# Kernel optimization log

Hardware: AMD Instinct MI355X
Metric: run time of the kernel (lower is better)

## Reference

```python
import jax, jax.numpy as jnp
import numpy as np

HEADS = 16
DIM_HEAD = 64
SCALE = DIM_HEAD ** -0.5


def setup_inputs() -> dict:
    key = jax.random.key(0)
    k1, k2, k3 = jax.random.split(key, 3)
    B, N, C = 2, 2048, 1024
    inner = HEADS * DIM_HEAD  # 1024
    x = jax.random.normal(k1, (B, N, C), dtype=jnp.float32)
    w_qkv = jax.random.normal(k2, (C, 3 * inner), dtype=jnp.float32) * (C ** -0.5)
    w_proj = jax.random.normal(k3, (inner, C), dtype=jnp.float32) * (inner ** -0.5)
    b_proj = jnp.zeros((C,), dtype=jnp.float32)
    return {"x": x, "w_qkv": w_qkv, "w_proj": w_proj, "b_proj": b_proj}


def reference(x, w_qkv, w_proj, b_proj):
    B, N, C = x.shape
    qkv = x @ w_qkv  # [B, N, 3*inner]
    qkv = qkv.reshape(B, N, 3, HEADS, DIM_HEAD)
    qkv = jnp.transpose(qkv, (2, 0, 3, 1, 4))  # [3, B, H, N, D]
    q, k, v = qkv[0], qkv[1], qkv[2]
    q = q * SCALE
    attn = jnp.einsum('bhnd,bhmd->bhnm', q, k)  # [B, H, N, N]
    attn = jax.nn.softmax(attn, axis=-1)
    out = jnp.einsum('bhnm,bhmd->bhnd', attn, v)  # [B, H, N, D]
    out = jnp.transpose(out, (0, 2, 1, 3)).reshape(B, N, HEADS * DIM_HEAD)
    return out @ w_proj + b_proj
```

## Files before the change

### kernel.cpp

```cpp
#include <hip/hip_runtime.h>
#include <hip/hip_bf16.h>
#include <cstdint>
#include <cstddef>

static constexpr int BATCH = 2;
static constexpr int SEQ   = 2048;
static constexpr int CDIM  = 1024;
static constexpr int ROWS  = BATCH * SEQ;
static constexpr int QKVN  = 3 * CDIM;

typedef short bf16x8 __attribute__((ext_vector_type(8)));
typedef short bf16x4 __attribute__((ext_vector_type(4)));
typedef float f32x4  __attribute__((ext_vector_type(4)));

__device__ inline short f2bf(float f) {
    union { float f; unsigned u; } v; v.f = f;
    unsigned u = v.u;
    u += 0x7fffu + ((u >> 16) & 1u);
    return (short)(u >> 16);
}

__device__ inline unsigned pk_bf16(float a, float b) {
    union { float f; unsigned u; } ua, ub;
    ua.f = a; ub.f = b;
    unsigned xa = ua.u + 0x7fffu + ((ua.u >> 16) & 1u);
    unsigned xb = ub.u + 0x7fffu + ((ub.u >> 16) & 1u);
    return __builtin_amdgcn_perm(xb, xa, 0x07060302);
}

__device__ inline void glds16(const short* g, short* l) {
    __builtin_amdgcn_global_load_lds(
        (const __attribute__((address_space(1))) void*)g,
        (__attribute__((address_space(3))) void*)l, 16, 0, 0);
}

__device__ inline f32x4 mfma16_bf16(bf16x4 a, bf16x4 b, f32x4 c) {
#if __has_builtin(__builtin_amdgcn_mfma_f32_16x16x16bf16_1k)
    return __builtin_amdgcn_mfma_f32_16x16x16bf16_1k(a, b, c, 0, 0, 0);
#else
    asm("v_mfma_f32_16x16x16_bf16 %0, %1, %2, %0" : "+v"(c) : "v"(a), "v"(b));
    return c;
#endif
}

__global__ __launch_bounds__(256) void cvt_f32_bf16(const float* __restrict__ in,
                                                    short* __restrict__ out, int n4) {
    int i = blockIdx.x * 256 + threadIdx.x;
    if (i >= n4) return;
    float4 f = ((const float4*)in)[i];
    uint2 o;
    o.x = pk_bf16(f.x, f.y);
    o.y = pk_bf16(f.z, f.w);
    ((uint2*)out)[i] = o;
}

__global__ __launch_bounds__(256) void cvt_transpose(const float* __restrict__ in,
                                                     short* __restrict__ out, int R, int C,
                                                     float scale, int srows) {
    __shared__ float tile[32][33];
    int tx = threadIdx.x & 31, ty = threadIdx.x >> 5;
    int r0 = blockIdx.y * 32, c0 = blockIdx.x * 32;
    #pragma unroll
    for (int i = 0; i < 4; i++)
        tile[ty + i * 8][tx] = in[(size_t)(r0 + ty + i * 8) * C + c0 + tx];
    __syncthreads();
    #pragma unroll
    for (int i = 0; i < 4; i++) {
        int orow = c0 + ty + i * 8;
        float sc = (orow < srows) ? scale : 1.0f;
        out[(size_t)orow * R + r0 + tx] = f2bf(tile[tx][ty + i * 8] * sc);
    }
}

__global__ __launch_bounds__(256) void v_transpose(const short* __restrict__ qkv,
                                                   short* __restrict__ vTg) {
    __shared__ short tile[32][33];
    int bh = blockIdx.z, b = bh >> 4, h = bh & 15;
    int n0 = blockIdx.x * 32, d0 = blockIdx.y * 32;
    int tx = threadIdx.x & 31, ty = threadIdx.x >> 5;
    const short* src = qkv + (size_t)(b * SEQ) * QKVN + 2048 + h * 64;
    #pragma unroll
    for (int i = 0; i < 4; i++)
        tile[ty + i * 8][tx] = src[(size_t)(n0 + ty + i * 8) * QKVN + d0 + tx];
    __syncthreads();
    short* dst = vTg + (size_t)bh * (64 * SEQ);
    #pragma unroll
    for (int i = 0; i < 4; i++)
        dst[(size_t)(d0 + ty + i * 8) * SEQ + n0 + tx] = tile[tx][ty + i * 8];
}

template<int BF16OUT>
__global__ __launch_bounds__(256) void gemm_bt(const short* __restrict__ A,
                                               const short* __restrict__ Bt,
                                               void* __restrict__ C,
                                               const float* __restrict__ bias,
                                               int M, int N, int K) {
    __shared__ __align__(16) short As[128 * 32];
    __shared__ __align__(16) short Bs[128 * 32];

    const int t = threadIdx.x, wave = t >> 6, lane = t & 63;
    const int l15 = lane & 15, quad = lane >> 4;
    const int wr = wave >> 1, wc = wave & 1;
    const int m0 = blockIdx.y * 128, n0 = blockIdx.x * 128;

    f32x4 acc[4][4] = {};

    const short* gA = A  + (size_t)(m0 + wave * 32 + (lane >> 2)) * K + (lane & 3) * 8;
    const short* gB = Bt + (size_t)(n0 + wave * 32 + (lane >> 2)) * K + (lane & 3) * 8;
    short* lA = &As[wave * 32 * 32];
    short* lB = &Bs[wave * 32 * 32];

    for (int k0 = 0; k0 < K; k0 += 32) {
        glds16(gA + k0,          lA);
        glds16(gA + 16 * K + k0, lA + 512);
        glds16(gB + k0,          lB);
        glds16(gB + 16 * K + k0, lB + 512);
        __syncthreads();

        bf16x8 af[4], bf[4];
        #pragma unroll
        for (int i = 0; i < 4; i++)
            af[i] = *(const bf16x8*)&As[(wr * 64 + i * 16 + l15) * 32 + quad * 8];
        #pragma unroll
        for (int j = 0; j < 4; j++)
            bf[j] = *(const bf16x8*)&Bs[(wc * 64 + j * 16 + l15) * 32 + quad * 8];
        #pragma unroll
        for (int i = 0; i < 4; i++)
            #pragma unroll
            for (int j = 0; j < 4; j++)
                acc[i][j] = __builtin_amdgcn_mfma_f32_16x16x32_bf16(af[i], bf[j], acc[i][j], 0, 0, 0);
        __syncthreads();
    }

    #pragma unroll
    for (int i = 0; i < 4; i++) {
        #pragma unroll
        for (int j = 0; j < 4; j++) {
            #pragma unroll
            for (int r = 0; r < 4; r++) {
                int row = m0 + wr * 64 + i * 16 + quad * 4 + r;
                int col = n0 + wc * 64 + j * 16 + l15;
                float v = acc[i][j][r];
                if (BF16OUT) ((short*)C)[(size_t)row * N + col] = f2bf(v);
                else         ((float*)C)[(size_t)row * N + col] = v + bias[col];
            }
        }
    }
}

static constexpr int KP      = 64 * 32;
static constexpr int VT_OFF  = 2 * KP;
static constexpr int LDV     = 72;
static constexpr int SMEM_SH = VT_OFF + 64 * LDV;

__global__ __launch_bounds__(256) void attn_kernel(const short* __restrict__ qkv,
                                                   const short* __restrict__ vTg,
                                                   short* __restrict__ attn_out) {
    __shared__ __align__(16) short smem[SMEM_SH];

    const int t = threadIdx.x, wave = t >> 6, lane = t & 63;
    const int l15 = lane & 15, quad = lane >> 4;
    const int bh = blockIdx.y, b = bh >> 4, h = bh & 15;
    const int q0 = blockIdx.x * 64;
    const size_t baseQ = (size_t)(b * SEQ) * QKVN + h * 64;

    const size_t qoff = baseQ + (size_t)(q0 + wave * 16 + l15) * QKVN + quad * 8;
    bf16x8 qf0 = *(const bf16x8*)&qkv[qoff];
    bf16x8 qf1 = *(const bf16x8*)&qkv[qoff + 32];

    const short* gK = qkv + baseQ + 1024
                    + (size_t)(wave * 16 + (lane >> 2)) * QKVN + (lane & 3) * 8;
    short* lK0 = smem + wave * 512;
    short* lK1 = smem + KP + wave * 512;

    const short* gV = vTg + (size_t)bh * (64 * SEQ);
    const int vd = t >> 3, vc = t & 7;

    float m_i = -INFINITY, l_i = 0.f;
    f32x4 ot[4] = {};

    for (int j0 = 0; j0 < SEQ; j0 += 64) {
        glds16(gK + (size_t)j0 * QKVN,      lK0);
        glds16(gK + (size_t)j0 * QKVN + 32, lK1);
        {
            int4 v0 = *(const int4*)&gV[(size_t)vd * SEQ + j0 + vc * 8];
            int4 v1 = *(const int4*)&gV[(size_t)(vd + 32) * SEQ + j0 + vc * 8];
            *(int4*)&smem[VT_OFF + vd * LDV + vc * 8]        = v0;
            *(int4*)&smem[VT_OFF + (vd + 32) * LDV + vc * 8] = v1;
        }
        __syncthreads();

        f32x4 s[4];
        #pragma unroll
        for (int sub = 0; sub < 4; sub++) {
            bf16x8 kf0 = *(const bf16x8*)&smem[(sub * 16 + l15) * 32 + quad * 8];
            bf16x8 kf1 = *(const bf16x8*)&smem[KP + (sub * 16 + l15) * 32 + quad * 8];
            f32x4 a = {};
            a = __builtin_amdgcn_mfma_f32_16x16x32_bf16(kf0, qf0, a, 0, 0, 0);
            a = __builtin_amdgcn_mfma_f32_16x16x32_bf16(kf1, qf1, a, 0, 0, 0);
            s[sub] = a;
        }

        float mx = fmaxf(fmaxf(fmaxf(s[0][0], s[0][1]), fmaxf(s[0][2], s[0][3])),
                         fmaxf(fmaxf(s[1][0], s[1][1]), fmaxf(s[1][2], s[1][3])));
        mx = fmaxf(mx, fmaxf(fmaxf(fmaxf(s[2][0], s[2][1]), fmaxf(s[2][2], s[2][3])),
                             fmaxf(fmaxf(s[3][0], s[3][1]), fmaxf(s[3][2], s[3][3]))));
        mx = fmaxf(mx, __shfl_xor(mx, 16));
        mx = fmaxf(mx, __shfl_xor(mx, 32));
        float mn = fmaxf(m_i, mx);
        if (!__all(mn == m_i)) {
            float alpha = __builtin_amdgcn_exp2f(m_i - mn);
            m_i = mn;
            l_i *= alpha;
            #pragma unroll
            for (int d = 0; d < 4; d++)
                #pragma unroll
                for (int r = 0; r < 4; r++) ot[d][r] *= alpha;
        }

        float rs = 0.f;
        #pragma unroll
        for (int sub = 0; sub < 4; sub++) {
            float p0 = __builtin_amdgcn_exp2f(s[sub][0] - m_i);
            float p1 = __builtin_amdgcn_exp2f(s[sub][1] - m_i);
            float p2 = __builtin_amdgcn_exp2f(s[sub][2] - m_i);
            float p3 = __builtin_amdgcn_exp2f(s[sub][3] - m_i);
            rs += (p0 + p1) + (p2 + p3);
            union { unsigned u[2]; bf16x4 v; } pu;
            pu.u[0] = pk_bf16(p0, p1);
            pu.u[1] = pk_bf16(p2, p3);
            #pragma unroll
            for (int d = 0; d < 4; d++) {
                bf16x4 vf = *(const bf16x4*)&smem[VT_OFF + (d * 16 + l15) * LDV
                                                 + sub * 16 + quad * 4];
                ot[d] = mfma16_bf16(vf, pu.v, ot[d]);
            }
        }
        rs += __shfl_xor(rs, 16);
        rs += __shfl_xor(rs, 32);
        l_i += rs;
        __syncthreads();
    }

    float inv = 1.0f / l_i;
    #pragma unroll
    for (int d = 0; d < 4; d++) {
        unsigned w0 = pk_bf16(ot[d][0] * inv, ot[d][1] * inv);
        unsigned w1 = pk_bf16(ot[d][2] * inv, ot[d][3] * inv);
        *(unsigned*)&smem[VT_OFF + (wave * 16 + l15) * LDV + d * 16 + quad * 4]     = w0;
        *(unsigned*)&smem[VT_OFF + (wave * 16 + l15) * LDV + d * 16 + quad * 4 + 2] = w1;
    }
    __syncthreads();
    {
        int row = t >> 3, ch = t & 7;
        #pragma unroll
        for (int p = 0; p < 2; p++) {
            int rr = row + p * 32;
            int4 v = *(const int4*)&smem[VT_OFF + rr * LDV + ch * 8];
            *(int4*)&attn_out[(size_t)(b * SEQ + q0 + rr) * CDIM + h * 64 + ch * 8] = v;
        }
    }
}

extern "C" void kernel_launch(void* const* d_in, const int* in_sizes, int n_in,
                              void* d_out, int out_size, void* d_ws, size_t ws_size,
                              hipStream_t stream) {
    const float* x      = (const float*)d_in[0];
    const float* w_qkv  = (const float*)d_in[1];
    const float* w_proj = (const float*)d_in[2];
    const float* b_proj = (const float*)d_in[3];
    float* out = (float*)d_out;

    char* ws = (char*)d_ws;
    short* x_bf    = (short*)(ws);
    short* wqkvT   = (short*)(ws + 8388608);
    short* wprojT  = (short*)(ws + 14680064);
    short* qkv_bf  = (short*)(ws + 16777216);
    short* attn_bf = (short*)(ws + 41943040);
    short* vTg     = x_bf;

    const float SMUL = 0.125f * 1.44269504088896340736f;

    cvt_f32_bf16<<<4096, 256, 0, stream>>>(x, x_bf, ROWS * CDIM / 4);
    cvt_transpose<<<dim3(QKVN / 32, CDIM / 32), 256, 0, stream>>>(w_qkv, wqkvT, CDIM, QKVN,
                                                                  SMUL, 1024);
    cvt_transpose<<<dim3(CDIM / 32, CDIM / 32), 256, 0, stream>>>(w_proj, wprojT, CDIM, CDIM,
                                                                  1.0f, 0);

    gemm_bt<1><<<dim3(QKVN / 128, ROWS / 128), 256, 0, stream>>>(
        x_bf, wqkvT, qkv_bf, nullptr, ROWS, QKVN, CDIM);

    v_transpose<<<dim3(SEQ / 32, 2, BATCH * 16), 256, 0, stream>>>(qkv_bf, vTg);

    attn_kernel<<<dim3(SEQ / 64, BATCH * 16), 256, 0, stream>>>(qkv_bf, vTg, attn_bf);

    gemm_bt<0><<<dim3(CDIM / 128, ROWS / 128), 256, 0, stream>>>(
        attn_bf, wprojT, out, b_proj, ROWS, CDIM, CDIM);
}
```

Measured before the change: 225.8 us.

## Widen attention KV tile, compute row sums via MFMA, shrink proj GEMM tile

The attention kernel now processes 128 keys per iteration instead of 64, which halves the number of loop iterations and barriers. The softmax row sum is now accumulated by an extra MFMA against a vector of ones instead of scalar adds and cross-lane shuffles. The output projection GEMM uses 64-row tiles, which doubles its block count so the small GEMM fills the GPU better. In exchange the kernel uses more shared memory and more registers for the larger score tile, and the row sum now comes from bf16-rounded probabilities.

```diff
diff --git a/kernel.cpp b/kernel.cpp
--- a/kernel.cpp
+++ b/kernel.cpp
@@ -89,43 +89,44 @@
         dst[(size_t)(d0 + ty + i * 8) * SEQ + n0 + tx] = tile[tx][ty + i * 8];
 }
 
-template<int BF16OUT>
+template<int BF16OUT, int MT>
 __global__ __launch_bounds__(256) void gemm_bt(const short* __restrict__ A,
                                                const short* __restrict__ Bt,
                                                void* __restrict__ C,
                                                const float* __restrict__ bias,
                                                int M, int N, int K) {
-    __shared__ __align__(16) short As[128 * 32];
+    constexpr int AF = MT / 32;
+    __shared__ __align__(16) short As[MT * 32];
     __shared__ __align__(16) short Bs[128 * 32];
 
     const int t = threadIdx.x, wave = t >> 6, lane = t & 63;
     const int l15 = lane & 15, quad = lane >> 4;
     const int wr = wave >> 1, wc = wave & 1;
-    const int m0 = blockIdx.y * 128, n0 = blockIdx.x * 128;
-
-    f32x4 acc[4][4] = {};
-
-    const short* gA = A  + (size_t)(m0 + wave * 32 + (lane >> 2)) * K + (lane & 3) * 8;
+    const int m0 = blockIdx.y * MT, n0 = blockIdx.x * 128;
+
+    f32x4 acc[AF][4] = {};
+
+    const short* gA = A  + (size_t)(m0 + wave * (MT / 4) + (lane >> 2)) * K + (lane & 3) * 8;
     const short* gB = Bt + (size_t)(n0 + wave * 32 + (lane >> 2)) * K + (lane & 3) * 8;
-    short* lA = &As[wave * 32 * 32];
+    short* lA = &As[wave * (MT / 4) * 32];
     short* lB = &Bs[wave * 32 * 32];
 
     for (int k0 = 0; k0 < K; k0 += 32) {
-        glds16(gA + k0,          lA);
-        glds16(gA + 16 * K + k0, lA + 512);
+        glds16(gA + k0, lA);
+        if constexpr (MT == 128) glds16(gA + 16 * K + k0, lA + 512);
         glds16(gB + k0,          lB);
         glds16(gB + 16 * K + k0, lB + 512);
         __syncthreads();
 
-        bf16x8 af[4], bf[4];
-        #pragma unroll
-        for (int i = 0; i < 4; i++)
-            af[i] = *(const bf16x8*)&As[(wr * 64 + i * 16 + l15) * 32 + quad * 8];
+        bf16x8 af[AF], bf[4];
+        #pragma unroll
+        for (int i = 0; i < AF; i++)
+            af[i] = *(const bf16x8*)&As[(wr * (MT / 2) + i * 16 + l15) * 32 + quad * 8];
         #pragma unroll
         for (int j = 0; j < 4; j++)
             bf[j] = *(const bf16x8*)&Bs[(wc * 64 + j * 16 + l15) * 32 + quad * 8];
         #pragma unroll
-        for (int i = 0; i < 4; i++)
+        for (int i = 0; i < AF; i++)
             #pragma unroll
             for (int j = 0; j < 4; j++)
                 acc[i][j] = __builtin_amdgcn_mfma_f32_16x16x32_bf16(af[i], bf[j], acc[i][j], 0, 0, 0);
@@ -133,12 +134,12 @@
     }
 
     #pragma unroll
-    for (int i = 0; i < 4; i++) {
+    for (int i = 0; i < AF; i++) {
         #pragma unroll
         for (int j = 0; j < 4; j++) {
             #pragma unroll
             for (int r = 0; r < 4; r++) {
-                int row = m0 + wr * 64 + i * 16 + quad * 4 + r;
+                int row = m0 + wr * (MT / 2) + i * 16 + quad * 4 + r;
                 int col = n0 + wc * 64 + j * 16 + l15;
                 float v = acc[i][j][r];
                 if (BF16OUT) ((short*)C)[(size_t)row * N + col] = f2bf(v);
@@ -148,9 +149,9 @@
     }
 }
 
-static constexpr int KP      = 64 * 32;
+static constexpr int KP      = 128 * 32;
 static constexpr int VT_OFF  = 2 * KP;
-static constexpr int LDV     = 72;
+static constexpr int LDV     = 136;
 static constexpr int SMEM_SH = VT_OFF + 64 * LDV;
 
 __global__ __launch_bounds__(256) void attn_kernel(const short* __restrict__ qkv,
@@ -169,30 +170,40 @@
     bf16x8 qf1 = *(const bf16x8*)&qkv[qoff + 32];
 
     const short* gK = qkv + baseQ + 1024
-                    + (size_t)(wave * 16 + (lane >> 2)) * QKVN + (lane & 3) * 8;
-    short* lK0 = smem + wave * 512;
-    short* lK1 = smem + KP + wave * 512;
+                    + (size_t)(wave * 32 + (lane >> 2)) * QKVN + (lane & 3) * 8;
+    short* lK0 = smem + wave * 1024;
+    short* lK1 = smem + KP + wave * 1024;
 
     const short* gV = vTg + (size_t)bh * (64 * SEQ);
     const int vd = t >> 3, vc = t & 7;
 
-    float m_i = -INFINITY, l_i = 0.f;
+    const bf16x4 ones = { (short)0x3F80, (short)0x3F80, (short)0x3F80, (short)0x3F80 };
+
+    float m_i = -INFINITY;
     f32x4 ot[4] = {};
-
-    for (int j0 = 0; j0 < SEQ; j0 += 64) {
-        glds16(gK + (size_t)j0 * QKVN,      lK0);
-        glds16(gK + (size_t)j0 * QKVN + 32, lK1);
+    f32x4 ol = {};
+
+    for (int j0 = 0; j0 < SEQ; j0 += 128) {
+        const size_t jadd = (size_t)j0 * QKVN;
+        glds16(gK + jadd,                       lK0);
+        glds16(gK + jadd + (size_t)16 * QKVN,   lK0 + 512);
+        glds16(gK + jadd + 32,                  lK1);
+        glds16(gK + jadd + (size_t)16 * QKVN + 32, lK1 + 512);
         {
-            int4 v0 = *(const int4*)&gV[(size_t)vd * SEQ + j0 + vc * 8];
-            int4 v1 = *(const int4*)&gV[(size_t)(vd + 32) * SEQ + j0 + vc * 8];
-            *(int4*)&smem[VT_OFF + vd * LDV + vc * 8]        = v0;
-            *(int4*)&smem[VT_OFF + (vd + 32) * LDV + vc * 8] = v1;
+            int4 v00 = *(const int4*)&gV[(size_t)vd * SEQ + j0 + vc * 8];
+            int4 v01 = *(const int4*)&gV[(size_t)vd * SEQ + j0 + 64 + vc * 8];
+            int4 v10 = *(const int4*)&gV[(size_t)(vd + 32) * SEQ + j0 + vc * 8];
+            int4 v11 = *(const int4*)&gV[(size_t)(vd + 32) * SEQ + j0 + 64 + vc * 8];
+            *(int4*)&smem[VT_OFF + vd * LDV + vc * 8]             = v00;
+            *(int4*)&smem[VT_OFF + vd * LDV + 64 + vc * 8]        = v01;
+            *(int4*)&smem[VT_OFF + (vd + 32) * LDV + vc * 8]      = v10;
+            *(int4*)&smem[VT_OFF + (vd + 32) * LDV + 64 + vc * 8] = v11;
         }
         __syncthreads();
 
-        f32x4 s[4];
-        #pragma unroll
-        for (int sub = 0; sub < 4; sub++) {
+        f32x4 s[8];
+        #pragma unroll
+        for (int sub = 0; sub < 8; sub++) {
             bf16x8 kf0 = *(const bf16x8*)&smem[(sub * 16 + l15) * 32 + quad * 8];
             bf16x8 kf1 = *(const bf16x8*)&smem[KP + (sub * 16 + l15) * 32 + quad * 8];
             f32x4 a = {};
@@ -201,34 +212,36 @@
             s[sub] = a;
         }
 
-        float mx = fmaxf(fmaxf(fmaxf(s[0][0], s[0][1]), fmaxf(s[0][2], s[0][3])),
-                         fmaxf(fmaxf(s[1][0], s[1][1]), fmaxf(s[1][2], s[1][3])));
-        mx = fmaxf(mx, fmaxf(fmaxf(fmaxf(s[2][0], s[2][1]), fmaxf(s[2][2], s[2][3])),
-                             fmaxf(fmaxf(s[3][0], s[3][1]), fmaxf(s[3][2], s[3][3]))));
+        float m4[8];
+        #pragma unroll
+        for (int sub = 0; sub < 8; sub++)
+            m4[sub] = fmaxf(fmaxf(s[sub][0], s[sub][1]), fmaxf(s[sub][2], s[sub][3]));
+        float mx = fmaxf(fmaxf(fmaxf(m4[0], m4[1]), fmaxf(m4[2], m4[3])),
+                         fmaxf(fmaxf(m4[4], m4[5]), fmaxf(m4[6], m4[7])));
         mx = fmaxf(mx, __shfl_xor(mx, 16));
         mx = fmaxf(mx, __shfl_xor(mx, 32));
         float mn = fmaxf(m_i, mx);
         if (!__all(mn == m_i)) {
             float alpha = __builtin_amdgcn_exp2f(m_i - mn);
             m_i = mn;
-            l_i *= alpha;
             #pragma unroll
-            for (int d = 0; d < 4; d++)
-                #pragma unroll
-                for (int r = 0; r < 4; r++) ot[d][r] *= alpha;
-        }
-
-        float rs = 0.f;
-        #pragma unroll
-        for (int sub = 0; sub < 4; sub++) {
+            for (int r = 0; r < 4; r++) {
+                ot[0][r] *= alpha; ot[1][r] *= alpha;
+                ot[2][r] *= alpha; ot[3][r] *= alpha;
+                ol[r]    *= alpha;
+            }
+        }
+
+        #pragma unroll
+        for (int sub = 0; sub < 8; sub++) {
             float p0 = __builtin_amdgcn_exp2f(s[sub][0] - m_i);
             float p1 = __builtin_amdgcn_exp2f(s[sub][1] - m_i);
             float p2 = __builtin_amdgcn_exp2f(s[sub][2] - m_i);
             float p3 = __builtin_amdgcn_exp2f(s[sub][3] - m_i);
-            rs += (p0 + p1) + (p2 + p3);
             union { unsigned u[2]; bf16x4 v; } pu;
             pu.u[0] = pk_bf16(p0, p1);
             pu.u[1] = pk_bf16(p2, p3);
+            ol = mfma16_bf16(ones, pu.v, ol);
             #pragma unroll
             for (int d = 0; d < 4; d++) {
                 bf16x4 vf = *(const bf16x4*)&smem[VT_OFF + (d * 16 + l15) * LDV
@@ -236,13 +249,10 @@
                 ot[d] = mfma16_bf16(vf, pu.v, ot[d]);
             }
         }
-        rs += __shfl_xor(rs, 16);
-        rs += __shfl_xor(rs, 32);
-        l_i += rs;
         __syncthreads();
     }
 
-    float inv = 1.0f / l_i;
+    float inv = 1.0f / ol[0];
     #pragma unroll
     for (int d = 0; d < 4; d++) {
         unsigned w0 = pk_bf16(ot[d][0] * inv, ot[d][1] * inv);
@@ -287,13 +297,13 @@
     cvt_transpose<<<dim3(CDIM / 32, CDIM / 32), 256, 0, stream>>>(w_proj, wprojT, CDIM, CDIM,
                                                                   1.0f, 0);
 
-    gemm_bt<1><<<dim3(QKVN / 128, ROWS / 128), 256, 0, stream>>>(
+    gemm_bt<1, 128><<<dim3(QKVN / 128, ROWS / 128), 256, 0, stream>>>(
         x_bf, wqkvT, qkv_bf, nullptr, ROWS, QKVN, CDIM);
 
     v_transpose<<<dim3(SEQ / 32, 2, BATCH * 16), 256, 0, stream>>>(qkv_bf, vTg);
 
     attn_kernel<<<dim3(SEQ / 64, BATCH * 16), 256, 0, stream>>>(qkv_bf, vTg, attn_bf);
 
-    gemm_bt<0><<<dim3(CDIM / 128, ROWS / 128), 256, 0, stream>>>(
+    gemm_bt<0, 64><<<dim3(CDIM / 128, ROWS / 64), 256, 0, stream>>>(
         attn_bf, wprojT, out, b_proj, ROWS, CDIM, CDIM);
 }
```

After: 216.5 us. 1.04x faster.
